# Optimization experiments

Measured on AMD Instinct MI355X. Metric: run time of the kernel, lower is better.

The kernel has to match this reference:

```python
import jax, jax.numpy as jnp
from jax import lax
import numpy as np

ROUTINGS = 3
NUM_CAPSULE = 8
NUM_ATOMS = 32

def _squash(x):
    # squash(x) = x/||x|| * ||x||^2/(1+||x||^2), norm over last axis
    norm = jnp.linalg.norm(x, axis=-1, keepdims=True)
    norm_sq = norm * norm
    return x / norm * (norm_sq / (1.0 + norm_sq))

def setup_inputs() -> dict:
    key = jax.random.key(0)
    k1, k2, k3 = jax.random.split(key, 3)
    input_tensor = jax.random.normal(k1, (2, 24, 24, 24, 8, 32), dtype=jnp.float32)
    # he_normal-ish scale for conv kernel [k,k,k,in_atoms, C*A]
    fan_in = 3 * 3 * 3 * 32
    W = jax.random.normal(k2, (3, 3, 3, 32, NUM_CAPSULE * NUM_ATOMS), dtype=jnp.float32) * np.sqrt(2.0 / fan_in).astype(np.float32)
    b = jnp.full((1, 1, 1, NUM_CAPSULE, NUM_ATOMS), 0.1, dtype=jnp.float32)
    return {"input_tensor": input_tensor, "W": W, "b": b}

def reference(input_tensor, W, b):
    B, H, Wd, T, IC, IA = input_tensor.shape
    C, A = NUM_CAPSULE, NUM_ATOMS
    # fold input capsule dim into batch: [IC, B, H, W, T, IA] -> [IC*B, H, W, T, IA]
    x = jnp.transpose(input_tensor, (4, 0, 1, 2, 3, 5)).reshape(IC * B, H, Wd, T, IA)
    conv = lax.conv_general_dilated(
        x, W, window_strides=(1, 1, 1), padding='SAME',
        dimension_numbers=('NDHWC', 'DHWIO', 'NDHWC'))  # [IC*B, H, W, T, C*A]
    # reshape exactly as the TF layer does (leading dims relabelled [B, IC])
    votes = conv.reshape(B, IC, H, Wd, T, C, A)
    biases = jnp.broadcast_to(b, (H, Wd, T, C, A))
    logits = jnp.zeros((B, IC, H, Wd, T, C), dtype=votes.dtype)
    activation = None
    for i in range(ROUTINGS):
        route = jax.nn.softmax(logits, axis=-1)                     # [B,IC,H,W,T,C]
        # sum over input capsules of route-weighted votes, plus bias
        preactivate = jnp.sum(route[..., None] * votes, axis=1) + biases  # [B,H,W,T,C,A]
        activation = _squash(preactivate)
        if i < ROUTINGS - 1:
            # agreement update (last-iteration update never affects output)
            distances = jnp.sum(votes * activation[:, None], axis=-1)  # [B,IC,H,W,T,C]
            logits = logits + distances
    return activation
```

## Files before the change

kernel.cpp:

```cpp
#include <hip/hip_runtime.h>
#include <math.h>


#define SPT 13824

typedef __attribute__((ext_vector_type(8))) _Float16 half8;
typedef __attribute__((ext_vector_type(4))) float f32x4;

__device__ __forceinline__ float redhalf(float v) {
  v += __shfl_xor(v, 16);
  v += __shfl_xor(v, 8);
  v += __shfl_xor(v, 4);
  v += __shfl_xor(v, 2);
  v += __shfl_xor(v, 1);
  return v;
}

__global__ void prep_W(const float* __restrict__ W, _Float16* __restrict__ Wh) {
  const int tap = blockIdx.x;
  #pragma unroll
  for (int rep = 0; rep < 4; ++rep) {
    const int idx = rep * 256 + threadIdx.x;
    const int cb = idx >> 6;
    const int kg = (idx >> 4) & 3;
    const int nr = idx & 15;
    const int n  = cb * 16 + nr;
    half8 o;
    #pragma unroll
    for (int j = 0; j < 8; ++j)
      o[j] = (_Float16)W[(tap * 32 + kg * 8 + j) * 256 + n];
    *(half8*)(Wh + tap * 8192 + idx * 8) = o;
  }
}

__global__ __launch_bounds__(256, 4)
void caps_mfma7(const float* __restrict__ xg, const _Float16* __restrict__ Wh,
                const float* __restrict__ bg, float* __restrict__ outg) {
  __shared__ __align__(16) unsigned char lds[35840];
  float* smV = (float*)lds;

  const int t    = threadIdx.x;
  const int lane = t & 63;
  const int w    = t >> 6;
  const int wg   = (blockIdx.x & 7) * 432 + (blockIdx.x >> 3);
  const int rbase = wg * 8;
  const int b2   = rbase / SPT;
  const int posb = rbase % SPT;
  const int z  = posb / 576;
  const int y  = (posb % 576) / 24;
  const int x0 = posb % 24;

  const bool stager = t < 240;
  const int sdy  = t / 80;
  const int srem = t % 80;
  const int sxs  = srem >> 3;
  const int sic  = srem & 7;
  const int sn   = b2 * 8 + sic;
  const int sbin = sn & 1;
  const int sicin = sn >> 1;
  const int syy  = y + sdy - 1;
  const int sxx  = x0 + sxs - 1;
  const int sR   = (sdy * 10 + sxs) * 8 + sic;
  const bool syx_ok = (unsigned)syy < 24u && (unsigned)sxx < 24u;
  const float* sbase = xg + (((sbin * 24) * 24 + (syx_ok ? syy : 0)) * 24 + (syx_ok ? sxx : 0)) * 256 + sicin * 32;

  const int lm = lane & 15;
  int abase[4];
  #pragma unroll
  for (int mi = 0; mi < 4; ++mi)
    abase[mi] = ((mi * 2 + (lm >> 3)) * 8 + (lane & 7)) * 72 + (lane >> 4) * 16;

  const _Float16* bbase = Wh + w * 2048 + lane * 8;

  f32x4 acc[4][4];
  #pragma unroll
  for (int mi = 0; mi < 4; ++mi)
    #pragma unroll
    for (int ni = 0; ni < 4; ++ni) acc[mi][ni] = (f32x4){0.f, 0.f, 0.f, 0.f};

  {
    const int zz = z - 1;
    const bool val = (unsigned)zz < 24u && syx_ok;
    const float* src = sbase + (zz >= 0 ? zz : 0) * 24 * 24 * 256;
    half8 h[4];
    #pragma unroll
    for (int j = 0; j < 4; ++j) {
      float4 qa = val ? *(const float4*)(src + j * 8)     : (float4){0,0,0,0};
      float4 qb = val ? *(const float4*)(src + j * 8 + 4) : (float4){0,0,0,0};
      half8 hh;
      hh[0]=(_Float16)qa.x; hh[1]=(_Float16)qa.y; hh[2]=(_Float16)qa.z; hh[3]=(_Float16)qa.w;
      hh[4]=(_Float16)qb.x; hh[5]=(_Float16)qb.y; hh[6]=(_Float16)qb.z; hh[7]=(_Float16)qb.w;
      h[j] = hh;
    }
    if (stager) {
      unsigned char* dst = lds + sR * 72;
      #pragma unroll
      for (int j = 0; j < 4; ++j) *(half8*)(dst + j * 16) = h[j];
    }
  }
  __syncthreads();

  #pragma unroll 1
  for (int dz = 0; dz < 3; ++dz) {
    half8 h[4];
    const bool have = dz < 2;
    {
      const int zz = z + dz;
      const bool val = have && (unsigned)zz < 24u && syx_ok;
      const float* src = sbase + zz * 24 * 24 * 256;
      #pragma unroll
      for (int j = 0; j < 4; ++j) {
        float4 qa = val ? *(const float4*)(src + j * 8)     : (float4){0,0,0,0};
        float4 qb = val ? *(const float4*)(src + j * 8 + 4) : (float4){0,0,0,0};
        half8 hh;
        hh[0]=(_Float16)qa.x; hh[1]=(_Float16)qa.y; hh[2]=(_Float16)qa.z; hh[3]=(_Float16)qa.w;
        hh[4]=(_Float16)qb.x; hh[5]=(_Float16)qb.y; hh[6]=(_Float16)qb.z; hh[7]=(_Float16)qb.w;
        h[j] = hh;
      }
    }

    const unsigned char* sb = lds + (dz & 1) * 17280;
    #pragma unroll 1
    for (int dy = 0; dy < 3; ++dy) {
      const _Float16* bt = bbase + (dz * 9 + dy * 3) * 8192;
      half8 bA0, bA1, bA2, bA3, bB0, bB1, bB2, bB3;
      bA0 = *(const half8*)(bt + 0 * 512);
      bA1 = *(const half8*)(bt + 1 * 512);
      bA2 = *(const half8*)(bt + 2 * 512);
      bA3 = *(const half8*)(bt + 3 * 512);

      bB0 = *(const half8*)(bt + 8192 + 0 * 512);
      bB1 = *(const half8*)(bt + 8192 + 1 * 512);
      bB2 = *(const half8*)(bt + 8192 + 2 * 512);
      bB3 = *(const half8*)(bt + 8192 + 3 * 512);
      {
        const int imm = dy * 5760;
        half8 af[4];
        #pragma unroll
        for (int mi = 0; mi < 4; ++mi) af[mi] = *(const half8*)(sb + abase[mi] + imm);
        #pragma unroll
        for (int mi = 0; mi < 4; ++mi) {
          acc[mi][0] = __builtin_amdgcn_mfma_f32_16x16x32_f16(af[mi], bA0, acc[mi][0], 0, 0, 0);
          acc[mi][1] = __builtin_amdgcn_mfma_f32_16x16x32_f16(af[mi], bA1, acc[mi][1], 0, 0, 0);
          acc[mi][2] = __builtin_amdgcn_mfma_f32_16x16x32_f16(af[mi], bA2, acc[mi][2], 0, 0, 0);
          acc[mi][3] = __builtin_amdgcn_mfma_f32_16x16x32_f16(af[mi], bA3, acc[mi][3], 0, 0, 0);
        }
      }
      bA0 = *(const half8*)(bt + 16384 + 0 * 512);
      bA1 = *(const half8*)(bt + 16384 + 1 * 512);
      bA2 = *(const half8*)(bt + 16384 + 2 * 512);
      bA3 = *(const half8*)(bt + 16384 + 3 * 512);
      {
        const int imm = dy * 5760 + 576;
        half8 af[4];
        #pragma unroll
        for (int mi = 0; mi < 4; ++mi) af[mi] = *(const half8*)(sb + abase[mi] + imm);
        #pragma unroll
        for (int mi = 0; mi < 4; ++mi) {
          acc[mi][0] = __builtin_amdgcn_mfma_f32_16x16x32_f16(af[mi], bB0, acc[mi][0], 0, 0, 0);
          acc[mi][1] = __builtin_amdgcn_mfma_f32_16x16x32_f16(af[mi], bB1, acc[mi][1], 0, 0, 0);
          acc[mi][2] = __builtin_amdgcn_mfma_f32_16x16x32_f16(af[mi], bB2, acc[mi][2], 0, 0, 0);
          acc[mi][3] = __builtin_amdgcn_mfma_f32_16x16x32_f16(af[mi], bB3, acc[mi][3], 0, 0, 0);
        }
      }
      {
        const int imm = dy * 5760 + 1152;
        half8 af[4];
        #pragma unroll
        for (int mi = 0; mi < 4; ++mi) af[mi] = *(const half8*)(sb + abase[mi] + imm);
        #pragma unroll
        for (int mi = 0; mi < 4; ++mi) {
          acc[mi][0] = __builtin_amdgcn_mfma_f32_16x16x32_f16(af[mi], bA0, acc[mi][0], 0, 0, 0);
          acc[mi][1] = __builtin_amdgcn_mfma_f32_16x16x32_f16(af[mi], bA1, acc[mi][1], 0, 0, 0);
          acc[mi][2] = __builtin_amdgcn_mfma_f32_16x16x32_f16(af[mi], bA2, acc[mi][2], 0, 0, 0);
          acc[mi][3] = __builtin_amdgcn_mfma_f32_16x16x32_f16(af[mi], bA3, acc[mi][3], 0, 0, 0);
        }
      }
    }

    if (have && stager) {
      unsigned char* dst = lds + ((dz + 1) & 1) * 17280 + sR * 72;
      #pragma unroll
      for (int j = 0; j < 4; ++j) *(half8*)(dst + j * 16) = h[j];
    }
    __syncthreads();
  }

  const int ch = lane >> 5;
  const int al = lane & 31;
  float* smLw = (float*)(lds + 33792) + w * 128;

  float bia[4];
  #pragma unroll
  for (int q = 0; q < 4; ++q) bia[q] = bg[(2 * q + ch) * 32 + al];

  #pragma unroll 1
  for (int pass = 0; pass < 2; ++pass) {
    #pragma unroll
    for (int mh = 0; mh < 2; ++mh) {
      const int mi = pass * 2 + mh;
      #pragma unroll
      for (int ni = 0; ni < 4; ++ni) {
        #pragma unroll
        for (int j = 0; j < 4; ++j) {
          const int rl  = mh * 16 + (lane >> 4) * 4 + j;
          const int col = w * 64 + ni * 16 + (lane & 15);
          smV[rl * 264 + col] = acc[mi][ni][j];
        }
      }
    }
    __syncthreads();

    float v[8][4];
    #pragma unroll
    for (int ic = 0; ic < 8; ++ic)
      #pragma unroll
      for (int q = 0; q < 4; ++q)
        v[ic][q] = smV[(w * 8 + ic) * 264 + (2 * q + ch) * 32 + al];

    #pragma unroll 1
    for (int it = 0; it < 3; ++it) {
      const float* Lrd = smLw + ((it + 1) & 1) * 64;
      float pre[4];
      #pragma unroll
      for (int q = 0; q < 4; ++q) pre[q] = bia[q];
      if (it == 0) {
        #pragma unroll
        for (int ic = 0; ic < 8; ++ic)
          #pragma unroll
          for (int q = 0; q < 4; ++q)
            pre[q] = fmaf(0.125f, v[ic][q], pre[q]);
      } else {
        #pragma unroll
        for (int ic = 0; ic < 8; ++ic) {
          float Lv[8];
          #pragma unroll
          for (int cc = 0; cc < 8; ++cc) Lv[cc] = Lrd[ic * 8 + cc];
          float mx = Lv[0];
          #pragma unroll
          for (int cc = 1; cc < 8; ++cc) mx = fmaxf(mx, Lv[cc]);
          float e[8];
          float s = 0.f;
          #pragma unroll
          for (int cc = 0; cc < 8; ++cc) { e[cc] = __expf(Lv[cc] - mx); s += e[cc]; }
          const float inv = 1.0f / s;
          #pragma unroll
          for (int q = 0; q < 4; ++q)
            pre[q] = fmaf(e[2 * q + ch] * inv, v[ic][q], pre[q]);
        }
      }

      float act[4];
      #pragma unroll
      for (int q = 0; q < 4; ++q) {
        float ns = redhalf(pre[q] * pre[q]);
        act[q] = pre[q] * (sqrtf(ns) / (1.0f + ns));
      }

      if (it == 2) {
        const int pl = pass * 4 + w;
        #pragma unroll
        for (int q = 0; q < 4; ++q)
          outg[(rbase + pl) * 256 + (2 * q + ch) * 32 + al] = act[q];
      } else {
        float d[8][4];
        #pragma unroll
        for (int ic = 0; ic < 8; ++ic)
          #pragma unroll
          for (int q = 0; q < 4; ++q)
            d[ic][q] = redhalf(v[ic][q] * act[q]);
        float* Lwr = smLw + (it & 1) * 64;
        if (al == 0) {
          #pragma unroll
          for (int ic = 0; ic < 8; ++ic)
            #pragma unroll
            for (int q = 0; q < 4; ++q) {
              const int cc = 2 * q + ch;
              Lwr[ic * 8 + cc] = (it == 0) ? d[ic][q] : Lrd[ic * 8 + cc] + d[ic][q];
            }
        }
        __syncthreads();
      }
    }
  }
}

__global__ __launch_bounds__(256, 3)
void caps_fused(const float* __restrict__ xg, const float* __restrict__ Wg,
                const float* __restrict__ bg, float* __restrict__ outg) {
  __shared__ __align__(16) float sm[10432];
  float* smA = sm;
  float* smB = sm + 2176;
  float* smV = sm;
  float* smL = sm + 10368;

  const int t    = threadIdx.x;
  const int blk  = blockIdx.x;
  const int rbase = blk * 8;
  const int b2   = rbase / SPT;
  const int posb = rbase % SPT;
  const int z  = posb / 576;
  const int y  = (posb % 576) / 24;
  const int x0 = posb % 24;

  const int pix_t = t >> 4;
  const int oc_t  = t & 15;
  const int am    = t >> 2;
  const int acin  = (t & 3) * 8;
  const int a_pl  = am >> 3;
  const int a_n   = b2 * 8 + (am & 7);
  const int a_bin = a_n & 1;
  const int a_icin = a_n >> 1;

  float acc[4][16];
  #pragma unroll
  for (int i = 0; i < 4; ++i)
    #pragma unroll
    for (int j = 0; j < 16; ++j) acc[i][j] = 0.f;

  #pragma unroll 1
  for (int tap = 0; tap < 27; ++tap) {
    const int dz = tap / 9, dy = (tap % 9) / 3, dx = tap % 3;
    const int zz = z + dz - 1;
    const int yy = y + dy - 1;
    const int xx = x0 + a_pl + dx - 1;

    float4 va = {0.f, 0.f, 0.f, 0.f}, vb = {0.f, 0.f, 0.f, 0.f};
    if ((unsigned)zz < 24u && (unsigned)yy < 24u && (unsigned)xx < 24u) {
      const float* src = xg + ((((a_bin * 24 + zz) * 24 + yy) * 24 + xx) * 8 + a_icin) * 32 + acin;
      va = *(const float4*)src;
      vb = *(const float4*)(src + 4);
    }
    float4 wv[8];
    const float* wsrc = Wg + tap * 8192 + t * 4;
    #pragma unroll
    for (int k = 0; k < 8; ++k) wv[k] = *(const float4*)(wsrc + k * 1024);

    __syncthreads();
    smA[(acin + 0) * 68 + am] = va.x;
    smA[(acin + 1) * 68 + am] = va.y;
    smA[(acin + 2) * 68 + am] = va.z;
    smA[(acin + 3) * 68 + am] = va.w;
    smA[(acin + 4) * 68 + am] = vb.x;
    smA[(acin + 5) * 68 + am] = vb.y;
    smA[(acin + 6) * 68 + am] = vb.z;
    smA[(acin + 7) * 68 + am] = vb.w;
    #pragma unroll
    for (int k = 0; k < 8; ++k) *(float4*)&smB[k * 1024 + t * 4] = wv[k];
    __syncthreads();

    #pragma unroll 8
    for (int cin = 0; cin < 32; ++cin) {
      const float4 a4  = *(const float4*)&smA[cin * 68 + pix_t * 4];
      const float4 b0  = *(const float4*)&smB[cin * 256 + oc_t * 4];
      const float4 b1  = *(const float4*)&smB[cin * 256 + oc_t * 4 + 64];
      const float4 b2v = *(const float4*)&smB[cin * 256 + oc_t * 4 + 128];
      const float4 b3v = *(const float4*)&smB[cin * 256 + oc_t * 4 + 192];
      const float ar[4] = {a4.x, a4.y, a4.z, a4.w};
      #pragma unroll
      for (int i = 0; i < 4; ++i) {
        acc[i][0]  = fmaf(ar[i], b0.x,  acc[i][0]);
        acc[i][1]  = fmaf(ar[i], b0.y,  acc[i][1]);
        acc[i][2]  = fmaf(ar[i], b0.z,  acc[i][2]);
        acc[i][3]  = fmaf(ar[i], b0.w,  acc[i][3]);
        acc[i][4]  = fmaf(ar[i], b1.x,  acc[i][4]);
        acc[i][5]  = fmaf(ar[i], b1.y,  acc[i][5]);
        acc[i][6]  = fmaf(ar[i], b1.z,  acc[i][6]);
        acc[i][7]  = fmaf(ar[i], b1.w,  acc[i][7]);
        acc[i][8]  = fmaf(ar[i], b2v.x, acc[i][8]);
        acc[i][9]  = fmaf(ar[i], b2v.y, acc[i][9]);
        acc[i][10] = fmaf(ar[i], b2v.z, acc[i][10]);
        acc[i][11] = fmaf(ar[i], b2v.w, acc[i][11]);
        acc[i][12] = fmaf(ar[i], b3v.x, acc[i][12]);
        acc[i][13] = fmaf(ar[i], b3v.y, acc[i][13]);
        acc[i][14] = fmaf(ar[i], b3v.z, acc[i][14]);
        acc[i][15] = fmaf(ar[i], b3v.w, acc[i][15]);
      }
    }
  }
  __syncthreads();

  const int c = t >> 5;
  const int a = t & 31;
  const float bia = bg[t];

  #pragma unroll 1
  for (int pass = 0; pass < 2; ++pass) {
    if ((pix_t >> 3) == pass) {
      const int rl = (pix_t & 7) * 4;
      #pragma unroll
      for (int i = 0; i < 4; ++i) {
        #pragma unroll
        for (int jj = 0; jj < 4; ++jj) {
          float4 v4 = {acc[i][jj * 4 + 0], acc[i][jj * 4 + 1],
                       acc[i][jj * 4 + 2], acc[i][jj * 4 + 3]};
          *(float4*)&smV[(rl + i) * 256 + oc_t * 4 + jj * 64] = v4;
        }
      }
    }
    __syncthreads();

    #pragma unroll 1
    for (int pp = 0; pp < 4; ++pp) {
      const int pl = pass * 4 + pp;
      float v[8];
      #pragma unroll
      for (int ic = 0; ic < 8; ++ic) v[ic] = smV[(pp * 8 + ic) * 256 + t];

      float route[8];
      #pragma unroll 1
      for (int it = 0; it < 3; ++it) {
        if (it == 0) {
          #pragma unroll
          for (int ic = 0; ic < 8; ++ic) route[ic] = 0.125f;
        } else {
          #pragma unroll
          for (int ic = 0; ic < 8; ++ic) {
            float mx = -3.4e38f;
            #pragma unroll
            for (int cc = 0; cc < 8; ++cc) mx = fmaxf(mx, smL[ic * 8 + cc]);
            float s = 0.f;
            #pragma unroll
            for (int cc = 0; cc < 8; ++cc) s += __expf(smL[ic * 8 + cc] - mx);
            route[ic] = __expf(smL[ic * 8 + c] - mx) / s;
          }
        }
        float pre = bia;
        #pragma unroll
        for (int ic = 0; ic < 8; ++ic) pre = fmaf(route[ic], v[ic], pre);

        float ns = redhalf(pre * pre);
        const float nrm = sqrtf(ns);
        const float act = pre * (nrm / (1.0f + ns));

        if (it == 2) {
          outg[(rbase + pl) * 256 + t] = act;
        } else {
          float d[8];
          #pragma unroll
          for (int ic = 0; ic < 8; ++ic) d[ic] = redhalf(v[ic] * act);
          __syncthreads();
          if (a == 0) {
            #pragma unroll
            for (int ic = 0; ic < 8; ++ic)
              smL[ic * 8 + c] = (it == 0) ? d[ic] : smL[ic * 8 + c] + d[ic];
          }
          __syncthreads();
        }
      }
    }
    __syncthreads();
  }
}

extern "C" void kernel_launch(void* const* d_in, const int* in_sizes, int n_in,
                              void* d_out, int out_size, void* d_ws, size_t ws_size,
                              hipStream_t stream) {
  const float* x = (const float*)d_in[0];
  const float* W = (const float*)d_in[1];
  const float* b = (const float*)d_in[2];
  float* out = (float*)d_out;
  (void)in_sizes; (void)n_in; (void)out_size;

  if (ws_size >= 27u * 8192u * sizeof(_Float16)) {
    _Float16* Wh = (_Float16*)d_ws;
    prep_W<<<dim3(27), dim3(256), 0, stream>>>(W, Wh);
    caps_mfma7<<<dim3(3456), dim3(256), 0, stream>>>(x, Wh, b, out);
  } else {
    caps_fused<<<dim3(3456), dim3(256), 0, stream>>>(x, W, b, out);
  }
}
```

Measured before the change: 354.9 us.

## Split fused conv+routing kernel into separate conv and routing kernels via fp16 workspace

Splits the fused kernel in two when the workspace is large enough. The conv kernel writes its fp16 votes to global workspace, and a separate routing kernel reads them back and runs the three routing iterations with one wavefront per position. The goal is to drop the LDS staging and occupancy limits that the routing epilogue placed on the MFMA conv. The cost is an extra global round trip of about 113 MB of fp16 votes, plus votes rounded to fp16 before routing; logit reads are also vectorised to float4.

```diff
diff --git a/kernel.cpp b/kernel.cpp
--- a/kernel.cpp
+++ b/kernel.cpp
@@ -34,10 +34,9 @@
 }
 
 __global__ __launch_bounds__(256, 4)
-void caps_mfma7(const float* __restrict__ xg, const _Float16* __restrict__ Wh,
-                const float* __restrict__ bg, float* __restrict__ outg) {
-  __shared__ __align__(16) unsigned char lds[35840];
-  float* smV = (float*)lds;
+void caps_conv(const float* __restrict__ xg, const _Float16* __restrict__ Wh,
+               _Float16* __restrict__ vws) {
+  __shared__ __align__(16) unsigned char lds[34560];
 
   const int t    = threadIdx.x;
   const int lane = t & 63;
@@ -186,6 +185,262 @@
     __syncthreads();
   }
 
+  _Float16* vb = vws + (size_t)wg * 64 * 256;
+  const int rowb = (lane >> 4) * 4;
+  const int colb = w * 64 + (lane & 15);
+  #pragma unroll
+  for (int mi = 0; mi < 4; ++mi)
+    #pragma unroll
+    for (int ni = 0; ni < 4; ++ni)
+      #pragma unroll
+      for (int j = 0; j < 4; ++j)
+        vb[(mi * 16 + rowb + j) * 256 + colb + ni * 16] = (_Float16)acc[mi][ni][j];
+}
+
+__global__ __launch_bounds__(256, 4)
+void caps_route(const _Float16* __restrict__ vws, const float* __restrict__ bg,
+                float* __restrict__ outg) {
+  __shared__ float smL[4 * 128];
+
+  const int t    = threadIdx.x;
+  const int lane = t & 63;
+  const int w    = t >> 6;
+  const int grow = blockIdx.x * 4 + w;
+
+  const int ch = lane >> 5;
+  const int al = lane & 31;
+  float* smLw = smL + w * 128;
+
+  float bia[4];
+  #pragma unroll
+  for (int q = 0; q < 4; ++q) bia[q] = bg[(2 * q + ch) * 32 + al];
+
+  const _Float16* vp = vws + (size_t)grow * 8 * 256;
+  float v[8][4];
+  #pragma unroll
+  for (int ic = 0; ic < 8; ++ic)
+    #pragma unroll
+    for (int q = 0; q < 4; ++q)
+      v[ic][q] = (float)vp[ic * 256 + (2 * q + ch) * 32 + al];
+
+  #pragma unroll 1
+  for (int it = 0; it < 3; ++it) {
+    const float* Lrd = smLw + ((it + 1) & 1) * 64;
+    float pre[4];
+    #pragma unroll
+    for (int q = 0; q < 4; ++q) pre[q] = bia[q];
+    if (it == 0) {
+      #pragma unroll
+      for (int ic = 0; ic < 8; ++ic)
+        #pragma unroll
+        for (int q = 0; q < 4; ++q)
+          pre[q] = fmaf(0.125f, v[ic][q], pre[q]);
+    } else {
+      #pragma unroll
+      for (int ic = 0; ic < 8; ++ic) {
+        const float4 La = *(const float4*)(Lrd + ic * 8);
+        const float4 Lb = *(const float4*)(Lrd + ic * 8 + 4);
+        const float Lv[8] = {La.x, La.y, La.z, La.w, Lb.x, Lb.y, Lb.z, Lb.w};
+        float mx = Lv[0];
+        #pragma unroll
+        for (int cc = 1; cc < 8; ++cc) mx = fmaxf(mx, Lv[cc]);
+        float e[8];
+        float s = 0.f;
+        #pragma unroll
+        for (int cc = 0; cc < 8; ++cc) { e[cc] = __expf(Lv[cc] - mx); s += e[cc]; }
+        const float inv = 1.0f / s;
+        #pragma unroll
+        for (int q = 0; q < 4; ++q)
+          pre[q] = fmaf(e[2 * q + ch] * inv, v[ic][q], pre[q]);
+      }
+    }
+
+    float act[4];
+    #pragma unroll
+    for (int q = 0; q < 4; ++q) {
+      float ns = redhalf(pre[q] * pre[q]);
+      act[q] = pre[q] * (sqrtf(ns) / (1.0f + ns));
+    }
+
+    if (it == 2) {
+      #pragma unroll
+      for (int q = 0; q < 4; ++q)
+        outg[(size_t)grow * 256 + (2 * q + ch) * 32 + al] = act[q];
+    } else {
+      float d[8][4];
+      #pragma unroll
+      for (int ic = 0; ic < 8; ++ic)
+        #pragma unroll
+        for (int q = 0; q < 4; ++q)
+          d[ic][q] = redhalf(v[ic][q] * act[q]);
+      float* Lwr = smLw + (it & 1) * 64;
+      if (al == 0) {
+        #pragma unroll
+        for (int ic = 0; ic < 8; ++ic)
+          #pragma unroll
+          for (int q = 0; q < 4; ++q) {
+            const int cc = 2 * q + ch;
+            Lwr[ic * 8 + cc] = (it == 0) ? d[ic][q] : Lrd[ic * 8 + cc] + d[ic][q];
+          }
+      }
+      __syncthreads();
+    }
+  }
+}
+
+__global__ __launch_bounds__(256, 4)
+void caps_mfma7(const float* __restrict__ xg, const _Float16* __restrict__ Wh,
+                const float* __restrict__ bg, float* __restrict__ outg) {
+  __shared__ __align__(16) unsigned char lds[35840];
+  float* smV = (float*)lds;
+
+  const int t    = threadIdx.x;
+  const int lane = t & 63;
+  const int w    = t >> 6;
+  const int wg   = (blockIdx.x & 7) * 432 + (blockIdx.x >> 3);
+  const int rbase = wg * 8;
+  const int b2   = rbase / SPT;
+  const int posb = rbase % SPT;
+  const int z  = posb / 576;
+  const int y  = (posb % 576) / 24;
+  const int x0 = posb % 24;
+
+  const bool stager = t < 240;
+  const int sdy  = t / 80;
+  const int srem = t % 80;
+  const int sxs  = srem >> 3;
+  const int sic  = srem & 7;
+  const int sn   = b2 * 8 + sic;
+  const int sbin = sn & 1;
+  const int sicin = sn >> 1;
+  const int syy  = y + sdy - 1;
+  const int sxx  = x0 + sxs - 1;
+  const int sR   = (sdy * 10 + sxs) * 8 + sic;
+  const bool syx_ok = (unsigned)syy < 24u && (unsigned)sxx < 24u;
+  const float* sbase = xg + (((sbin * 24) * 24 + (syx_ok ? syy : 0)) * 24 + (syx_ok ? sxx : 0)) * 256 + sicin * 32;
+
+  const int lm = lane & 15;
+  int abase[4];
+  #pragma unroll
+  for (int mi = 0; mi < 4; ++mi)
+    abase[mi] = ((mi * 2 + (lm >> 3)) * 8 + (lane & 7)) * 72 + (lane >> 4) * 16;
+
+  const _Float16* bbase = Wh + w * 2048 + lane * 8;
+
+  f32x4 acc[4][4];
+  #pragma unroll
+  for (int mi = 0; mi < 4; ++mi)
+    #pragma unroll
+    for (int ni = 0; ni < 4; ++ni) acc[mi][ni] = (f32x4){0.f, 0.f, 0.f, 0.f};
+
+  {
+    const int zz = z - 1;
+    const bool val = (unsigned)zz < 24u && syx_ok;
+    const float* src = sbase + (zz >= 0 ? zz : 0) * 24 * 24 * 256;
+    half8 h[4];
+    #pragma unroll
+    for (int j = 0; j < 4; ++j) {
+      float4 qa = val ? *(const float4*)(src + j * 8)     : (float4){0,0,0,0};
+      float4 qb = val ? *(const float4*)(src + j * 8 + 4) : (float4){0,0,0,0};
+      half8 hh;
+      hh[0]=(_Float16)qa.x; hh[1]=(_Float16)qa.y; hh[2]=(_Float16)qa.z; hh[3]=(_Float16)qa.w;
+      hh[4]=(_Float16)qb.x; hh[5]=(_Float16)qb.y; hh[6]=(_Float16)qb.z; hh[7]=(_Float16)qb.w;
+      h[j] = hh;
+    }
+    if (stager) {
+      unsigned char* dst = lds + sR * 72;
+      #pragma unroll
+      for (int j = 0; j < 4; ++j) *(half8*)(dst + j * 16) = h[j];
+    }
+  }
+  __syncthreads();
+
+  #pragma unroll 1
+  for (int dz = 0; dz < 3; ++dz) {
+    half8 h[4];
+    const bool have = dz < 2;
+    {
+      const int zz = z + dz;
+      const bool val = have && (unsigned)zz < 24u && syx_ok;
+      const float* src = sbase + zz * 24 * 24 * 256;
+      #pragma unroll
+      for (int j = 0; j < 4; ++j) {
+        float4 qa = val ? *(const float4*)(src + j * 8)     : (float4){0,0,0,0};
+        float4 qb = val ? *(const float4*)(src + j * 8 + 4) : (float4){0,0,0,0};
+        half8 hh;
+        hh[0]=(_Float16)qa.x; hh[1]=(_Float16)qa.y; hh[2]=(_Float16)qa.z; hh[3]=(_Float16)qa.w;
+        hh[4]=(_Float16)qb.x; hh[5]=(_Float16)qb.y; hh[6]=(_Float16)qb.z; hh[7]=(_Float16)qb.w;
+        h[j] = hh;
+      }
+    }
+
+    const unsigned char* sb = lds + (dz & 1) * 17280;
+    #pragma unroll 1
+    for (int dy = 0; dy < 3; ++dy) {
+      const _Float16* bt = bbase + (dz * 9 + dy * 3) * 8192;
+      half8 bA0, bA1, bA2, bA3, bB0, bB1, bB2, bB3;
+      bA0 = *(const half8*)(bt + 0 * 512);
+      bA1 = *(const half8*)(bt + 1 * 512);
+      bA2 = *(const half8*)(bt + 2 * 512);
+      bA3 = *(const half8*)(bt + 3 * 512);
+
+      bB0 = *(const half8*)(bt + 8192 + 0 * 512);
+      bB1 = *(const half8*)(bt + 8192 + 1 * 512);
+      bB2 = *(const half8*)(bt + 8192 + 2 * 512);
+      bB3 = *(const half8*)(bt + 8192 + 3 * 512);
+      {
+        const int imm = dy * 5760;
+        half8 af[4];
+        #pragma unroll
+        for (int mi = 0; mi < 4; ++mi) af[mi] = *(const half8*)(sb + abase[mi] + imm);
+        #pragma unroll
+        for (int mi = 0; mi < 4; ++mi) {
+          acc[mi][0] = __builtin_amdgcn_mfma_f32_16x16x32_f16(af[mi], bA0, acc[mi][0], 0, 0, 0);
+          acc[mi][1] = __builtin_amdgcn_mfma_f32_16x16x32_f16(af[mi], bA1, acc[mi][1], 0, 0, 0);
+          acc[mi][2] = __builtin_amdgcn_mfma_f32_16x16x32_f16(af[mi], bA2, acc[mi][2], 0, 0, 0);
+          acc[mi][3] = __builtin_amdgcn_mfma_f32_16x16x32_f16(af[mi], bA3, acc[mi][3], 0, 0, 0);
+        }
+      }
+      bA0 = *(const half8*)(bt + 16384 + 0 * 512);
+      bA1 = *(const half8*)(bt + 16384 + 1 * 512);
+      bA2 = *(const half8*)(bt + 16384 + 2 * 512);
+      bA3 = *(const half8*)(bt + 16384 + 3 * 512);
+      {
+        const int imm = dy * 5760 + 576;
+        half8 af[4];
+        #pragma unroll
+        for (int mi = 0; mi < 4; ++mi) af[mi] = *(const half8*)(sb + abase[mi] + imm);
+        #pragma unroll
+        for (int mi = 0; mi < 4; ++mi) {
+          acc[mi][0] = __builtin_amdgcn_mfma_f32_16x16x32_f16(af[mi], bB0, acc[mi][0], 0, 0, 0);
+          acc[mi][1] = __builtin_amdgcn_mfma_f32_16x16x32_f16(af[mi], bB1, acc[mi][1], 0, 0, 0);
+          acc[mi][2] = __builtin_amdgcn_mfma_f32_16x16x32_f16(af[mi], bB2, acc[mi][2], 0, 0, 0);
+          acc[mi][3] = __builtin_amdgcn_mfma_f32_16x16x32_f16(af[mi], bB3, acc[mi][3], 0, 0, 0);
+        }
+      }
+      {
+        const int imm = dy * 5760 + 1152;
+        half8 af[4];
+        #pragma unroll
+        for (int mi = 0; mi < 4; ++mi) af[mi] = *(const half8*)(sb + abase[mi] + imm);
+        #pragma unroll
+        for (int mi = 0; mi < 4; ++mi) {
+          acc[mi][0] = __builtin_amdgcn_mfma_f32_16x16x32_f16(af[mi], bA0, acc[mi][0], 0, 0, 0);
+          acc[mi][1] = __builtin_amdgcn_mfma_f32_16x16x32_f16(af[mi], bA1, acc[mi][1], 0, 0, 0);
+          acc[mi][2] = __builtin_amdgcn_mfma_f32_16x16x32_f16(af[mi], bA2, acc[mi][2], 0, 0, 0);
+          acc[mi][3] = __builtin_amdgcn_mfma_f32_16x16x32_f16(af[mi], bA3, acc[mi][3], 0, 0, 0);
+        }
+      }
+    }
+
+    if (have && stager) {
+      unsigned char* dst = lds + ((dz + 1) & 1) * 17280 + sR * 72;
+      #pragma unroll
+      for (int j = 0; j < 4; ++j) *(half8*)(dst + j * 16) = h[j];
+    }
+    __syncthreads();
+  }
+
   const int ch = lane >> 5;
   const int al = lane & 31;
   float* smLw = (float*)(lds + 33792) + w * 128;
@@ -233,9 +488,9 @@
       } else {
         #pragma unroll
         for (int ic = 0; ic < 8; ++ic) {
-          float Lv[8];
-          #pragma unroll
-          for (int cc = 0; cc < 8; ++cc) Lv[cc] = Lrd[ic * 8 + cc];
+          const float4 La = *(const float4*)(Lrd + ic * 8);
+          const float4 Lb = *(const float4*)(Lrd + ic * 8 + 4);
+          const float Lv[8] = {La.x, La.y, La.z, La.w, Lb.x, Lb.y, Lb.z, Lb.w};
           float mx = Lv[0];
           #pragma unroll
           for (int cc = 1; cc < 8; ++cc) mx = fmaxf(mx, Lv[cc]);
@@ -462,7 +717,16 @@
   float* out = (float*)d_out;
   (void)in_sizes; (void)n_in; (void)out_size;
 
-  if (ws_size >= 27u * 8192u * sizeof(_Float16)) {
+  const size_t need_wh    = 27u * 8192u * sizeof(_Float16);
+  const size_t need_split = need_wh + (size_t)27648 * 2048 * sizeof(_Float16);
+
+  if (ws_size >= need_split) {
+    _Float16* Wh  = (_Float16*)d_ws;
+    _Float16* vws = (_Float16*)((unsigned char*)d_ws + need_wh);
+    prep_W<<<dim3(27), dim3(256), 0, stream>>>(W, Wh);
+    caps_conv<<<dim3(3456), dim3(256), 0, stream>>>(x, Wh, vws);
+    caps_route<<<dim3(6912), dim3(256), 0, stream>>>(vws, b, out);
+  } else if (ws_size >= need_wh) {
     _Float16* Wh = (_Float16*)d_ws;
     prep_W<<<dim3(27), dim3(256), 0, stream>>>(W, Wh);
     caps_mfma7<<<dim3(3456), dim3(256), 0, stream>>>(x, Wh, b, out);
```

Result: faster. 328.7 us (-7.4%).
